# Kernel optimization log

Measured on AMD Instinct MI355X. Metric: run time of the kernel, lower is better.

## Reference

```python
import jax, jax.numpy as jnp
import numpy as np
import math

ROPE_BASE = 10000.0
ALIBI_SLOPE = 2.0 ** (-8.0)  # _get_alibi_slopes(1) == [2**(-8*1/1)]


def _rope_cos_sin(T, d):
    inv_freq = 1.0 / (ROPE_BASE ** (jnp.arange(0, d, 2, dtype=jnp.float32) / d))
    t = jnp.arange(T, dtype=jnp.float32)
    freqs = jnp.einsum('i,j->ij', t, inv_freq)          # [T, d/2]
    emb = jnp.concatenate([freqs, freqs], axis=-1)      # [T, d]
    return jnp.cos(emb), jnp.sin(emb)


def _rotate_half(x):
    x1, x2 = jnp.split(x, 2, axis=-1)
    return jnp.concatenate([-x2, x1], axis=-1)


def setup_inputs() -> dict:
    key = jax.random.key(0)
    kq, kk, kv = jax.random.split(key, 3)
    B, T, H = 8, 2048, 256
    return {
        'q': jax.random.normal(kq, (B, T, H), dtype=jnp.float32),
        'k': jax.random.normal(kk, (B, T, H), dtype=jnp.float32),
        'v': jax.random.normal(kv, (B, T, H), dtype=jnp.float32),
    }


def reference(q, k, v):
    B, T, H = q.shape  # num_heads == 1, so head_dim == H
    cos, sin = _rope_cos_sin(T, H)                      # [T, H]
    qe = q * cos + _rotate_half(q) * sin                # [B, T, H]
    ke = k * cos + _rotate_half(k) * sin                # [B, T, H]

    scale = 1.0 / math.sqrt(H)
    scores = jnp.einsum('btd,bsd->bts', qe, ke) * scale  # [B, T, T]

    pos = jnp.arange(T)
    rel = (pos[None, :] - pos[:, None]).astype(jnp.float32)  # [T, T]
    alibi = (ALIBI_SLOPE * rel)[None, None, :, :]            # [1, 1, T, T]

    # torch broadcast: [B,T,T] + [1,1,T,T] -> [1,B,T,T]
    scores = scores + alibi
    attn = jax.nn.softmax(scores, axis=-1)              # [1, B, T, T]
    out = jnp.matmul(attn, v)                           # [1, B, T, H]
    return out
```

## Files before the change

### kernel.cpp

```cpp
#include <hip/hip_runtime.h>

#define B_ 8
#define T_ 2048
#define H_ 256
#define PSTR 72
#define SCALE2 0.0901684403f
#define SLOPE2 0.00563552752f
#define ELEMS ((size_t)B_ * T_ * H_)

typedef __attribute__((ext_vector_type(8))) short bf16x8;
typedef __attribute__((ext_vector_type(4))) float f32x4;

#define MFMA16(a, b, c) __builtin_amdgcn_mfma_f32_16x16x32_bf16((a), (b), (c), 0, 0, 0)

__device__ __forceinline__ ushort f2bf(float f) {
  unsigned u = __float_as_uint(f);
  u += 0x7FFFu + ((u >> 16) & 1u);
  return (ushort)(u >> 16);
}

__device__ __forceinline__ void gl_lds16(const ushort* g, ushort* l) {
  __builtin_amdgcn_global_load_lds(
      (const __attribute__((address_space(1))) unsigned int*)g,
      (__attribute__((address_space(3))) unsigned int*)l, 16, 0, 0);
}

__global__ void prep_kernel(const float* __restrict__ k, const float* __restrict__ v,
                            ushort* __restrict__ kt, ushort* __restrict__ vt) {
  __shared__ ushort tile[64][72];
  const int bid = blockIdx.x;
  const int tid = threadIdx.x;
  if (bid < 1024) {
    int idx = bid * 256 + tid;
    int d8 = idx & 15;
    int bt = idx >> 4;
    int t = bt & (T_ - 1);
    int b = bt >> 11;
    size_t base = (size_t)bt * H_ + d8 * 8;
    float4 a0 = *(const float4*)(k + base);
    float4 a1 = *(const float4*)(k + base + 4);
    float4 c0 = *(const float4*)(k + base + 128);
    float4 c1 = *(const float4*)(k + base + 132);
    float av[8] = {a0.x, a0.y, a0.z, a0.w, a1.x, a1.y, a1.z, a1.w};
    float cv[8] = {c0.x, c0.y, c0.z, c0.w, c1.x, c1.y, c1.z, c1.w};
    bf16x8 lo, hi;
#pragma unroll
    for (int e = 0; e < 8; ++e) {
      int j = d8 * 8 + e;
      float rv = (float)t * exp2f((float)j * -0.103810252959f) * 0.15915494309f;
      float fr = rv - floorf(rv);
      float sn = __builtin_amdgcn_sinf(fr), cs = __builtin_amdgcn_cosf(fr);
      lo[e] = (short)f2bf(av[e] * cs - cv[e] * sn);
      hi[e] = (short)f2bf(cv[e] * cs + av[e] * sn);
    }
    size_t kdst = (((size_t)(b * 64 + (t >> 5)) * 32 + d8) * 32 + (t & 31)) * 8;
    *(bf16x8*)(kt + kdst) = lo;
    *(bf16x8*)(kt + kdst + 4096) = hi;
  } else {
    int bid2 = bid - 1024;
    int b = bid2 >> 7, rem = bid2 & 127;
    int h0 = (rem >> 5) * 64, t0 = (rem & 31) * 64;
    int c4 = tid & 15, r0 = tid >> 4;
#pragma unroll
    for (int p = 0; p < 4; ++p) {
      int row = r0 + p * 16;
      const float4 f = *(const float4*)(v + ((size_t)(b * T_ + t0 + row)) * H_ + h0 + c4 * 4);
      ushort4 u;
      u.x = f2bf(f.x); u.y = f2bf(f.y); u.z = f2bf(f.z); u.w = f2bf(f.w);
      *(ushort4*)&tile[row][(c4 * 4) ^ (8 * ((row >> 3) & 7))] = u;
    }
    __syncthreads();
#pragma unroll
    for (int p = 0; p < 2; ++p) {
      int c = tid + p * 256;
      int h = c >> 3, tc = (c & 7) * 8;
      int xo = 8 * (c & 7);
      ushort4 u0, u1;
      u0.x = tile[tc + 0][h ^ xo]; u0.y = tile[tc + 1][h ^ xo];
      u0.z = tile[tc + 2][h ^ xo]; u0.w = tile[tc + 3][h ^ xo];
      u1.x = tile[tc + 4][h ^ xo]; u1.y = tile[tc + 5][h ^ xo];
      u1.z = tile[tc + 6][h ^ xo]; u1.w = tile[tc + 7][h ^ xo];
      int tg = t0 + tc;
      size_t dst = (((size_t)(b * 64 + (tg >> 5)) * 4 + ((tg >> 3) & 3)) * 256 + (h0 + h)) * 8;
      *(ushort4*)(vt + dst) = u0;
      *(ushort4*)(vt + dst + 4) = u1;
    }
  }
}

__global__ __launch_bounds__(512, 2)
void attn_kernel(const float* __restrict__ q, const ushort* __restrict__ kt,
                 const ushort* __restrict__ vt, float* __restrict__ out,
                 float* __restrict__ o1, float* __restrict__ lpart) {
  __shared__ ushort Ksh[2][16384];
  __shared__ ushort Vsh[2][16384];
  __shared__ ushort Psh[8][16 * PSTR];

  const int tid = threadIdx.x;
  const int w = tid >> 6, lane = tid & 63, quad = lane >> 4, l16 = lane & 15;
  const int b = blockIdx.x;
  const int q0 = blockIdx.y * 128;
  const int sp = blockIdx.z;
  const int kvb = sp * (T_ / 2);
  const int niter = 16;

  bf16x8 aq[8];
  {
    const float* qb = q + ((size_t)(b * T_) + q0 + w * 16) * H_;
    const int t = q0 + w * 16 + l16;
    float qv[8][8];
#pragma unroll
    for (int ks = 0; ks < 8; ++ks) {
      float4 x0 = *(const float4*)(qb + (size_t)l16 * H_ + ks * 32 + quad * 8);
      float4 x1 = *(const float4*)(qb + (size_t)l16 * H_ + ks * 32 + quad * 8 + 4);
      qv[ks][0] = x0.x; qv[ks][1] = x0.y; qv[ks][2] = x0.z; qv[ks][3] = x0.w;
      qv[ks][4] = x1.x; qv[ks][5] = x1.y; qv[ks][6] = x1.z; qv[ks][7] = x1.w;
    }
#pragma unroll
    for (int ks = 0; ks < 4; ++ks)
#pragma unroll
      for (int e = 0; e < 8; ++e) {
        int d = ks * 32 + quad * 8 + e;
        float rv = (float)t * exp2f((float)d * -0.103810252959f) * 0.15915494309f;
        float fr = rv - floorf(rv);
        float sn = __builtin_amdgcn_sinf(fr), cs = __builtin_amdgcn_cosf(fr);
        aq[ks][e]     = (short)f2bf(qv[ks][e] * cs - qv[ks + 4][e] * sn);
        aq[ks + 4][e] = (short)f2bf(qv[ks + 4][e] * cs + qv[ks][e] * sn);
      }
  }

  const f32x4 fzero = {0.f, 0.f, 0.f, 0.f};
  f32x4 O[16], lac = fzero;
#pragma unroll
  for (int ht = 0; ht < 16; ++ht) O[ht] = fzero;
  bf16x8 vones;
#pragma unroll
  for (int i = 0; i < 8; ++i) vones[i] = (short)0x3F80;

  const ushort* ktb = kt + (size_t)(b * 64 + sp * 32) * 8192;
  const ushort* vtb = vt + (size_t)(b * 64 + sp * 32) * 8192;
  const int stoff = tid * 8;

#pragma unroll
  for (int tt = 0; tt < 2; ++tt) {
    const ushort* kg = ktb + (size_t)tt * 16384;
    const ushort* vg = vtb + (size_t)tt * 16384;
#pragma unroll
    for (int i = 0; i < 4; ++i) {
      gl_lds16(kg + stoff + i * 4096, &Ksh[tt][stoff + i * 4096]);
      gl_lds16(vg + stoff + i * 4096, &Vsh[tt][stoff + i * 4096]);
    }
  }

  const float arb = SLOPE2 * (float)(q0 + w * 16 + quad * 4);

  for (int it = 0; it < niter; ++it) {
    const int p = it & 1;
    __builtin_amdgcn_sched_barrier(0);
    if (it == niter - 1) __builtin_amdgcn_s_waitcnt(0x0070);
    else                 __builtin_amdgcn_s_waitcnt(0x0F78);
    __builtin_amdgcn_s_barrier();
    __builtin_amdgcn_sched_barrier(0);

    f32x4 s[4] = {fzero, fzero, fzero, fzero};
#pragma unroll
    for (int ks = 0; ks < 8; ++ks)
#pragma unroll
      for (int nt = 0; nt < 4; ++nt) {
        bf16x8 kf = *(const bf16x8*)&Ksh[p][(nt >> 1) * 8192 +
            ((ks * 4 + quad) * 32 + (nt & 1) * 16 + l16) * 8];
        s[nt] = MFMA16(aq[ks], kf, s[nt]);
      }

#pragma unroll
    for (int nt = 0; nt < 4; ++nt) {
      float ac = SLOPE2 * (float)(kvb + it * 64 + nt * 16 + l16);
#pragma unroll
      for (int r = 0; r < 4; ++r) {
        float a0 = ac - arb - SLOPE2 * (float)r;
        float pv = __builtin_amdgcn_exp2f(fmaf(s[nt][r], SCALE2, a0));
        Psh[w][(quad * 4 + r) * PSTR + nt * 16 + l16] = f2bf(pv);
      }
    }

    bf16x8 pf0 = *(const bf16x8*)&Psh[w][l16 * PSTR + quad * 8];
    bf16x8 pf1 = *(const bf16x8*)&Psh[w][l16 * PSTR + 32 + quad * 8];
    lac = MFMA16(pf0, vones, lac);
    lac = MFMA16(pf1, vones, lac);
#pragma unroll
    for (int ht = 0; ht < 16; ++ht) {
      bf16x8 vf0 = *(const bf16x8*)&Vsh[p][(quad * 256 + ht * 16 + l16) * 8];
      bf16x8 vf1 = *(const bf16x8*)&Vsh[p][8192 + (quad * 256 + ht * 16 + l16) * 8];
      O[ht] = MFMA16(pf0, vf0, O[ht]);
      O[ht] = MFMA16(pf1, vf1, O[ht]);
    }

    __builtin_amdgcn_sched_barrier(0);
    __builtin_amdgcn_s_waitcnt(0xC07F);
    __builtin_amdgcn_s_barrier();
    __builtin_amdgcn_sched_barrier(0);

    if (it < niter - 2) {
      const ushort* kg = ktb + (size_t)(it + 2) * 16384;
      const ushort* vg = vtb + (size_t)(it + 2) * 16384;
#pragma unroll
      for (int i = 0; i < 4; ++i) {
        gl_lds16(kg + stoff + i * 4096, &Ksh[p][stoff + i * 4096]);
        gl_lds16(vg + stoff + i * 4096, &Vsh[p][stoff + i * 4096]);
      }
    }
  }

  float* od = (sp == 0) ? out : o1;
  float* ob = od + ((size_t)(b * T_) + q0 + w * 16) * H_;
#pragma unroll
  for (int r = 0; r < 4; ++r) {
    int row = quad * 4 + r;
#pragma unroll
    for (int ht = 0; ht < 16; ++ht)
      ob[(size_t)row * H_ + ht * 16 + l16] = O[ht][r];
  }
  if (l16 == 0) {
#pragma unroll
    for (int r = 0; r < 4; ++r)
      lpart[(size_t)(sp * B_ + b) * T_ + q0 + w * 16 + quad * 4 + r] = lac[r];
  }
}

__global__ void combine_kernel(float* __restrict__ out, const float* __restrict__ o1,
                               const float* __restrict__ lpart) {
  int idx = blockIdx.x * 256 + threadIdx.x;
  int row = idx >> 6;
  float inv = 1.0f / (lpart[row] + lpart[B_ * T_ + row]);
  float4 a = ((const float4*)out)[idx];
  float4 c = ((const float4*)o1)[idx];
  a.x = (a.x + c.x) * inv; a.y = (a.y + c.y) * inv;
  a.z = (a.z + c.z) * inv; a.w = (a.w + c.w) * inv;
  ((float4*)out)[idx] = a;
}

extern "C" void kernel_launch(void* const* d_in, const int* in_sizes, int n_in,
                              void* d_out, int out_size, void* d_ws, size_t ws_size,
                              hipStream_t stream) {
  const float* q = (const float*)d_in[0];
  const float* k = (const float*)d_in[1];
  const float* v = (const float*)d_in[2];
  float* out = (float*)d_out;

  ushort* kt = (ushort*)d_ws;
  ushort* vt = kt + ELEMS;
  float* o1 = (float*)(vt + ELEMS);
  float* lpart = o1 + ELEMS;

  prep_kernel<<<dim3(2048), 256, 0, stream>>>(k, v, kt, vt);
  attn_kernel<<<dim3(B_, T_ / 128, 2), 512, 0, stream>>>(q, kt, vt, out, o1, lpart);
  combine_kernel<<<dim3((B_ * T_ * H_ / 4) / 256), 256, 0, stream>>>(out, o1, lpart);
}
```

Baseline: 145.5 us.

## Software-pipeline QK^T one tile ahead of softmax and PV in attention loop

Restructures the main KV loop so the QK^T scores for tile it are computed while the exp/softmax and PV MFMAs consume the scores from tile it-1, with a prologue and epilogue. K and V loads are now staggered, with K prefetched two tiles ahead and V one tile ahead, and the waitcnt values are adjusted to match. The aim is to overlap the score MFMAs with the exponentials and the PV work and to hide load latency. In exchange it keeps an extra set of score registers live, which raises register pressure, and the hand-tuned waitcnt counts must be exactly right.

```diff
diff --git a/kernel.cpp b/kernel.cpp
--- a/kernel.cpp
+++ b/kernel.cpp
@@ -142,43 +142,71 @@
   const int stoff = tid * 8;
 
 #pragma unroll
-  for (int tt = 0; tt < 2; ++tt) {
-    const ushort* kg = ktb + (size_t)tt * 16384;
-    const ushort* vg = vtb + (size_t)tt * 16384;
-#pragma unroll
-    for (int i = 0; i < 4; ++i) {
-      gl_lds16(kg + stoff + i * 4096, &Ksh[tt][stoff + i * 4096]);
-      gl_lds16(vg + stoff + i * 4096, &Vsh[tt][stoff + i * 4096]);
-    }
-  }
+  for (int i = 0; i < 4; ++i)
+    gl_lds16(ktb + stoff + i * 4096, &Ksh[0][stoff + i * 4096]);
+  __builtin_amdgcn_sched_barrier(0);
+#pragma unroll
+  for (int i = 0; i < 4; ++i)
+    gl_lds16(ktb + 16384 + stoff + i * 4096, &Ksh[1][stoff + i * 4096]);
+  __builtin_amdgcn_sched_barrier(0);
+#pragma unroll
+  for (int i = 0; i < 4; ++i)
+    gl_lds16(vtb + stoff + i * 4096, &Vsh[0][stoff + i * 4096]);
 
   const float arb = SLOPE2 * (float)(q0 + w * 16 + quad * 4);
-
-  for (int it = 0; it < niter; ++it) {
+  f32x4 s_prev[4] = {fzero, fzero, fzero, fzero};
+
+  {
+    __builtin_amdgcn_sched_barrier(0);
+    __builtin_amdgcn_s_waitcnt(0x0F78);
+    __builtin_amdgcn_s_barrier();
+    __builtin_amdgcn_sched_barrier(0);
+#pragma unroll
+    for (int ks = 0; ks < 8; ++ks)
+#pragma unroll
+      for (int nt = 0; nt < 4; ++nt) {
+        bf16x8 kf = *(const bf16x8*)&Ksh[0][(nt >> 1) * 8192 +
+            ((ks * 4 + quad) * 32 + (nt & 1) * 16 + l16) * 8];
+        s_prev[nt] = MFMA16(aq[ks], kf, s_prev[nt]);
+      }
+    __builtin_amdgcn_sched_barrier(0);
+    __builtin_amdgcn_s_waitcnt(0xC07F);
+    __builtin_amdgcn_s_barrier();
+    __builtin_amdgcn_sched_barrier(0);
+#pragma unroll
+    for (int i = 0; i < 4; ++i)
+      gl_lds16(ktb + (size_t)2 * 16384 + stoff + i * 4096, &Ksh[0][stoff + i * 4096]);
+    __builtin_amdgcn_sched_barrier(0);
+#pragma unroll
+    for (int i = 0; i < 4; ++i)
+      gl_lds16(vtb + (size_t)1 * 16384 + stoff + i * 4096, &Vsh[1][stoff + i * 4096]);
+  }
+
+  for (int it = 1; it < niter; ++it) {
     const int p = it & 1;
     __builtin_amdgcn_sched_barrier(0);
-    if (it == niter - 1) __builtin_amdgcn_s_waitcnt(0x0070);
+    if (it == niter - 1) __builtin_amdgcn_s_waitcnt(0x0F74);
     else                 __builtin_amdgcn_s_waitcnt(0x0F78);
     __builtin_amdgcn_s_barrier();
     __builtin_amdgcn_sched_barrier(0);
 
-    f32x4 s[4] = {fzero, fzero, fzero, fzero};
+    f32x4 s_cur[4] = {fzero, fzero, fzero, fzero};
 #pragma unroll
     for (int ks = 0; ks < 8; ++ks)
 #pragma unroll
       for (int nt = 0; nt < 4; ++nt) {
         bf16x8 kf = *(const bf16x8*)&Ksh[p][(nt >> 1) * 8192 +
             ((ks * 4 + quad) * 32 + (nt & 1) * 16 + l16) * 8];
-        s[nt] = MFMA16(aq[ks], kf, s[nt]);
+        s_cur[nt] = MFMA16(aq[ks], kf, s_cur[nt]);
       }
 
 #pragma unroll
     for (int nt = 0; nt < 4; ++nt) {
-      float ac = SLOPE2 * (float)(kvb + it * 64 + nt * 16 + l16);
+      float ac = SLOPE2 * (float)(kvb + (it - 1) * 64 + nt * 16 + l16);
 #pragma unroll
       for (int r = 0; r < 4; ++r) {
         float a0 = ac - arb - SLOPE2 * (float)r;
-        float pv = __builtin_amdgcn_exp2f(fmaf(s[nt][r], SCALE2, a0));
+        float pv = __builtin_amdgcn_exp2f(fmaf(s_prev[nt][r], SCALE2, a0));
         Psh[w][(quad * 4 + r) * PSTR + nt * 16 + l16] = f2bf(pv);
       }
     }
@@ -189,12 +217,15 @@
     lac = MFMA16(pf1, vones, lac);
 #pragma unroll
     for (int ht = 0; ht < 16; ++ht) {
-      bf16x8 vf0 = *(const bf16x8*)&Vsh[p][(quad * 256 + ht * 16 + l16) * 8];
-      bf16x8 vf1 = *(const bf16x8*)&Vsh[p][8192 + (quad * 256 + ht * 16 + l16) * 8];
+      bf16x8 vf0 = *(const bf16x8*)&Vsh[1 - p][(quad * 256 + ht * 16 + l16) * 8];
+      bf16x8 vf1 = *(const bf16x8*)&Vsh[1 - p][8192 + (quad * 256 + ht * 16 + l16) * 8];
       O[ht] = MFMA16(pf0, vf0, O[ht]);
       O[ht] = MFMA16(pf1, vf1, O[ht]);
     }
 
+#pragma unroll
+    for (int nt = 0; nt < 4; ++nt) s_prev[nt] = s_cur[nt];
+
     __builtin_amdgcn_sched_barrier(0);
     __builtin_amdgcn_s_waitcnt(0xC07F);
     __builtin_amdgcn_s_barrier();
@@ -202,12 +233,44 @@
 
     if (it < niter - 2) {
       const ushort* kg = ktb + (size_t)(it + 2) * 16384;
-      const ushort* vg = vtb + (size_t)(it + 2) * 16384;
-#pragma unroll
-      for (int i = 0; i < 4; ++i) {
+#pragma unroll
+      for (int i = 0; i < 4; ++i)
         gl_lds16(kg + stoff + i * 4096, &Ksh[p][stoff + i * 4096]);
-        gl_lds16(vg + stoff + i * 4096, &Vsh[p][stoff + i * 4096]);
-      }
+    }
+    __builtin_amdgcn_sched_barrier(0);
+    if (it < niter - 1) {
+      const ushort* vg = vtb + (size_t)(it + 1) * 16384;
+#pragma unroll
+      for (int i = 0; i < 4; ++i)
+        gl_lds16(vg + stoff + i * 4096, &Vsh[1 - p][stoff + i * 4096]);
+    }
+  }
+
+  {
+    __builtin_amdgcn_sched_barrier(0);
+    __builtin_amdgcn_s_waitcnt(0x0070);
+    __builtin_amdgcn_s_barrier();
+    __builtin_amdgcn_sched_barrier(0);
+#pragma unroll
+    for (int nt = 0; nt < 4; ++nt) {
+      float ac = SLOPE2 * (float)(kvb + (niter - 1) * 64 + nt * 16 + l16);
+#pragma unroll
+      for (int r = 0; r < 4; ++r) {
+        float a0 = ac - arb - SLOPE2 * (float)r;
+        float pv = __builtin_amdgcn_exp2f(fmaf(s_prev[nt][r], SCALE2, a0));
+        Psh[w][(quad * 4 + r) * PSTR + nt * 16 + l16] = f2bf(pv);
+      }
+    }
+    bf16x8 pf0 = *(const bf16x8*)&Psh[w][l16 * PSTR + quad * 8];
+    bf16x8 pf1 = *(const bf16x8*)&Psh[w][l16 * PSTR + 32 + quad * 8];
+    lac = MFMA16(pf0, vones, lac);
+    lac = MFMA16(pf1, vones, lac);
+#pragma unroll
+    for (int ht = 0; ht < 16; ++ht) {
+      bf16x8 vf0 = *(const bf16x8*)&Vsh[1][(quad * 256 + ht * 16 + l16) * 8];
+      bf16x8 vf1 = *(const bf16x8*)&Vsh[1][8192 + (quad * 256 + ht * 16 + l16) * 8];
+      O[ht] = MFMA16(pf0, vf0, O[ht]);
+      O[ht] = MFMA16(pf1, vf1, O[ht]);
     }
   }
 
```

Result: no change. 144.9 us (-0.4%).
